# Kernel optimization log

Hardware: AMD Instinct MI355X
Metric: run time of the kernel (lower is better)

## Reference

```python
import jax, jax.numpy as jnp
import numpy as np

N, CAMS = 1, 4
C1, C2, NH = 256, 256, 8
H1, H2, W2 = 128, 64, 400
H, W = 128, 128


def setup_inputs() -> dict:
    key = jax.random.key(0)
    ks = jax.random.split(key, 16)
    sc = 0.02
    th = jax.random.uniform(ks[3], (N, CAMS)) * 2.0 * np.pi
    c, s = jnp.cos(th), jnp.sin(th)
    z, o = jnp.zeros_like(c), jnp.ones_like(c)
    rots = jnp.stack([jnp.stack([c, -s, z], -1), jnp.stack([s, c, z], -1), jnp.stack([z, z, o], -1)], -2)
    return {
        "list_a": jax.random.normal(ks[0], (N, C1, H, W), jnp.float32),
        "list_b": jax.random.normal(ks[1], (N * CAMS, C2, H2, W2), jnp.float32),
        "fov_list": jax.random.uniform(ks[2], (N, CAMS)) * 0.5 + 1.0,
        "rots_list": rots.astype(jnp.float32),
        "trans_list": jax.random.normal(ks[4], (N, CAMS, 3), jnp.float32),
        "fxs": jax.random.uniform(ks[5], (N, CAMS)) * 100.0 + 500.0,
        "cxs": jax.random.uniform(ks[6], (N, CAMS)) * 20.0 + 390.0,
        "pos_a": jax.random.normal(ks[7], (1, H1, C1), jnp.float32),
        "pos_b": jax.random.normal(ks[8], (1, H2, C2), jnp.float32),
        "Wq": jax.random.normal(ks[9], (C1, C1), jnp.float32) * sc,
        "bq": jnp.zeros((C1,), jnp.float32),
        "Wk": jax.random.normal(ks[10], (C1, C2), jnp.float32) * sc,
        "bk": jnp.zeros((C1,), jnp.float32),
        "Wv": jax.random.normal(ks[11], (C1, C2), jnp.float32) * sc,
        "bv": jnp.zeros((C1,), jnp.float32),
        "in_w": jax.random.normal(ks[12], (3 * C1, C1), jnp.float32) * sc,
        "in_b": jnp.zeros((3 * C1,), jnp.float32),
        "out_w": jax.random.normal(ks[13], (C1, C1), jnp.float32) * sc,
        "out_b": jnp.zeros((C1,), jnp.float32),
    }


def _polar_coords(w1, h1, Hh, Ww, rots, fx, cx):
    # per-pixel viewing angles from intrinsics (original image width hard-coded 800)
    pi = jnp.arange(w1, dtype=jnp.float32)
    pw = 800.0 / w1
    ang = jnp.arctan((pi * pw + pw / 2.0 - cx) / fx)
    R90 = jnp.array([[0.0, 1.0], [-1.0, 0.0]], jnp.float32)
    rot = R90 @ rots[:2, :2].astype(jnp.float32)
    cr, sr = rot[0, 0], rot[1, 0]
    ca = cr * jnp.cos(ang) + sr * jnp.sin(ang)
    sa = -sr * jnp.cos(ang) + cr * jnp.sin(ang)
    cxp = jnp.float32(Ww // 2)
    cyp = jnp.float32(Hh // 2)
    rmax = jnp.sqrt(cxp ** 2 + cyp ** 2)
    radii = jnp.linspace(0.0, 1.0, h1).reshape(h1, 1) * rmax
    x = cxp + radii * ca  # [h1, w1]
    y = cyp - radii * sa
    return x, y


def _bilinear(img, x, y):
    # img [C,H,W]; x,y pixel coords [h1,w1]; grid_sample(align_corners=True) after clamping
    Hh, Ww = img.shape[1], img.shape[2]
    x = jnp.clip(x, 0.0, Ww - 1.0)
    y = jnp.clip(y, 0.0, Hh - 1.0)
    x0 = jnp.floor(x); y0 = jnp.floor(y)
    x1 = jnp.clip(x0 + 1.0, 0.0, Ww - 1.0)
    y1 = jnp.clip(y0 + 1.0, 0.0, Hh - 1.0)
    wx = x - x0; wy = y - y0
    x0i, x1i = x0.astype(jnp.int32), x1.astype(jnp.int32)
    y0i, y1i = y0.astype(jnp.int32), y1.astype(jnp.int32)
    v00 = img[:, y0i, x0i]; v01 = img[:, y0i, x1i]
    v10 = img[:, y1i, x0i]; v11 = img[:, y1i, x1i]
    return v00 * (1 - wx) * (1 - wy) + v01 * wx * (1 - wy) + v10 * (1 - wx) * wy + v11 * wx * wy


def _mha(q, k, v, in_w, in_b, out_w, out_b, nh):
    E = q.shape[-1]
    dh = E // nh
    qq = q @ in_w[:E].T + in_b[:E]
    kk = k @ in_w[E:2 * E].T + in_b[E:2 * E]
    vv = v @ in_w[2 * E:].T + in_b[2 * E:]
    B, Lq, _ = q.shape
    Lk = k.shape[1]
    qq = qq.reshape(B, Lq, nh, dh)
    kk = kk.reshape(B, Lk, nh, dh)
    vv = vv.reshape(B, Lk, nh, dh)
    att = jnp.einsum('bqhd,bkhd->bhqk', qq, kk) / jnp.sqrt(jnp.float32(dh))
    p = jax.nn.softmax(att, axis=-1)
    o = jnp.einsum('bhqk,bkhd->bqhd', p, vv).reshape(B, Lq, E)
    return o @ out_w.T + out_b


def _forward(list_a, list_b, rots_list, fxs, cxs, pos_a, pos_b,
             Wq, bq, Wk, bk, Wv, bv, in_w, in_b, out_w, out_b):
    outs = []
    for i in range(list_a.shape[0]):
        a = list_a[i]
        C1_, h1, Wb = a.shape
        Hb = h1
        enh = None
        for j in (0, 3):  # cameras 1 and 2 are skipped by the original `continue`
            b = list_b[i * CAMS + j]
            C2_, h2, w2 = b.shape
            x, y = _polar_coords(w2, h1, a.shape[1], a.shape[2], rots_list[i, j], fxs[i, j], cxs[i, j])
            a_rect = _bilinear(a, x, y)                     # [C1, h1, w2]
            a_seq = jnp.transpose(a_rect, (2, 1, 0)) + pos_a  # [w2, h1, C1]
            b_seq = jnp.transpose(b, (2, 1, 0)) + pos_b       # [w2, h2, C2]
            q = a_seq @ Wq.T + bq
            k = b_seq @ Wk.T + bk
            v = b_seq @ Wv.T + bv
            o = _mha(q, k, v, in_w, in_b, out_w, out_b, NH)
            a_enh = jnp.transpose(o, (2, 1, 0))              # [C1, h1, w2]
            # scatter-add restore with nearest-pixel indices
            xi = jnp.clip(jnp.round(x), 0, a.shape[2] - 1).astype(jnp.int32)
            yi = jnp.clip(jnp.round(y), 0, a.shape[1] - 1).astype(jnp.int32)
            idx = (yi * a.shape[2] + xi).reshape(-1)
            vals = a_enh.reshape(C1_, -1)
            rest = jnp.zeros((C1_, a.shape[1] * a.shape[2]), a.dtype).at[:, idx].add(vals)
            cnt = jnp.zeros((a.shape[1] * a.shape[2],), a.dtype).at[idx].add(1.0)
            cnt = jnp.where(cnt == 0, 1.0, cnt)
            enh = (rest / cnt).reshape(a.shape)
            a = a + enh
        outs.append(a + enh)  # original double-adds the last camera's enhancement
    return jnp.stack(outs)


def reference(list_a, list_b, fov_list, rots_list, trans_list, fxs, cxs, pos_a, pos_b,
              Wq, bq, Wk, bk, Wv, bv, in_w, in_b, out_w, out_b):
    # fov_list / trans_list are accepted but unused in the original math path
    return _forward(list_a, list_b, rots_list, fxs, cxs, pos_a, pos_b,
                    Wq, bq, Wk, bk, Wv, bv, in_w, in_b, out_w, out_b)
```

## Files before the change

### kernel.cpp

```cpp
#include <hip/hip_runtime.h>

#define PIX 16384
#define MS 51200
#define MB 25600

typedef __attribute__((ext_vector_type(8))) short short8;
typedef __attribute__((ext_vector_type(4))) float floatx4;

__device__ inline ushort f2b(float x) {
  uint u = __float_as_uint(x);
  return (ushort)((u + 0x7fffu + ((u >> 16) & 1u)) >> 16);
}
__device__ inline float b2f(ushort u) {
  return __uint_as_float(((uint)u) << 16);
}

__global__ __launch_bounds__(256) void coords_kernel(
    const float* __restrict__ rots, const float* __restrict__ fxs,
    const float* __restrict__ cxs,
    float* __restrict__ xarr, float* __restrict__ yarr,
    int* __restrict__ idxarr, float* __restrict__ cnt)
{
  int jz = blockIdx.y;
  int j = jz ? 3 : 0;
  int s = blockIdx.x * 256 + threadIdx.x;
  int h = s / 400;
  int w = s - h * 400;
  float fx = fxs[j], cx = cxs[j];
  const float* R = rots + j * 9;
  float cr = R[3];
  float sr = -R[0];
  float t = (2.0f * (float)w + 1.0f - cx) / fx;
  float inv = 1.0f / sqrtf(1.0f + t * t);
  float ca = (cr + sr * t) * inv;
  float sa = (cr * t - sr) * inv;
  float rad = ((float)h * (1.0f / 127.0f)) * 90.50966799187808f;
  float x = 64.0f + rad * ca;
  float y = 64.0f - rad * sa;
  xarr[jz * MS + s] = x;
  yarr[jz * MS + s] = y;
  int xi = (int)fminf(fmaxf(rintf(x), 0.0f), 127.0f);
  int yi = (int)fminf(fmaxf(rintf(y), 0.0f), 127.0f);
  int pix = yi * 128 + xi;
  idxarr[jz * MS + s] = pix;
  atomicAdd(&cnt[jz * PIX + pix], 1.0f);
}

__global__ __launch_bounds__(256) void prefix_kernel(
    const float* __restrict__ cntg, int* __restrict__ offsetsg)
{
  const float* cnt = cntg + blockIdx.x * PIX;
  int* offsets = offsetsg + blockIdx.x * PIX;
  __shared__ int sh[256];
  int t = threadIdx.x;
  int base = t * 64;
  const float4* cp = (const float4*)(cnt + base);
  int sum = 0;
#pragma unroll
  for (int i = 0; i < 16; ++i) {
    float4 v = cp[i];
    sum += (int)v.x + (int)v.y + (int)v.z + (int)v.w;
  }
  sh[t] = sum;
  __syncthreads();
  for (int d = 1; d < 256; d <<= 1) {
    int v = (t >= d) ? sh[t - d] : 0;
    __syncthreads();
    sh[t] += v;
    __syncthreads();
  }
  int run = sh[t] - sum;
  int4* op = (int4*)(offsets + base);
#pragma unroll
  for (int i = 0; i < 16; ++i) {
    float4 v = cp[i];
    int a0 = (int)v.x, a1 = (int)v.y, a2 = (int)v.z, a3 = (int)v.w;
    int4 o;
    o.x = run; o.y = run + a0; o.z = run + a0 + a1; o.w = run + a0 + a1 + a2;
    op[i] = o;
    run += a0 + a1 + a2 + a3;
  }
}

__global__ __launch_bounds__(256) void fill_kernel(
    const int* __restrict__ idxarr, const int* __restrict__ offsets,
    int* __restrict__ cursor, int* __restrict__ order, int* __restrict__ pixs)
{
  int jz = blockIdx.y;
  int s = blockIdx.x * 256 + threadIdx.x;
  int pix = idxarr[jz * MS + s];
  int pos = offsets[jz * PIX + pix] + atomicAdd(&cursor[jz * PIX + pix], 1);
  order[jz * MS + pos] = (s % 400) * 128 + (s / 400);
  pixs[jz * MS + pos] = pix;
}

__global__ __launch_bounds__(256) void transpose_kernel(
    const float* __restrict__ src, ushort* __restrict__ dst)
{
  __shared__ float tile[64][65];
  int p0 = blockIdx.x * 64;
  int c0 = blockIdx.y * 64;
  int t = threadIdx.x;
  int pr = (t & 15) * 4;
  int cr = t >> 4;
#pragma unroll
  for (int q = 0; q < 4; ++q) {
    int c = cr + q * 16;
    float4 v = *(const float4*)(src + (size_t)(c0 + c) * PIX + p0 + pr);
    tile[pr + 0][c] = v.x;
    tile[pr + 1][c] = v.y;
    tile[pr + 2][c] = v.z;
    tile[pr + 3][c] = v.w;
  }
  __syncthreads();
  int p = t >> 2;
  int ch = (t & 3) * 16;
  ushort tmp[16];
#pragma unroll
  for (int i = 0; i < 16; ++i) tmp[i] = f2b(tile[p][ch + i]);
  ushort* d = dst + (size_t)(p0 + p) * 256 + c0 + ch;
  *(uint4*)(d) = *(uint4*)tmp;
  *(uint4*)(d + 8) = *(uint4*)(tmp + 8);
}

__global__ __launch_bounds__(256) void f2b_kernel(
    const float* __restrict__ in, ushort* __restrict__ out)
{
  int t = blockIdx.x * 256 + threadIdx.x;
  float4 v = ((const float4*)in)[t];
  ushort4 o;
  o.x = f2b(v.x); o.y = f2b(v.y); o.z = f2b(v.z); o.w = f2b(v.w);
  ((ushort4*)out)[t] = o;
}

#define LFP 264
__global__ __launch_bounds__(256) void sampleproj_kernel(
    const ushort* __restrict__ aT, const float* __restrict__ xarr,
    const float* __restrict__ yarr, const ushort* __restrict__ Wh,
    const float* __restrict__ bias, ushort* __restrict__ qh)
{
  __shared__ ushort lf[64 * LFP];
  int s0 = blockIdx.x * 64;
  int tid = threadIdx.x;
  int lane = tid & 63;
  int wave = tid >> 6;
  int col = lane & 15, quad = lane >> 4;
  int c0 = lane * 4;

#pragma unroll 4
  for (int i = 0; i < 16; ++i) {
    int sl = wave * 16 + i;
    int s = s0 + sl;
    float x = fminf(fmaxf(xarr[s], 0.0f), 127.0f);
    float y = fminf(fmaxf(yarr[s], 0.0f), 127.0f);
    float x0f = floorf(x), y0f = floorf(y);
    int x0 = (int)x0f, y0 = (int)y0f;
    int x1 = min(x0 + 1, 127), y1 = min(y0 + 1, 127);
    float wx = x - x0f, wy = y - y0f;
    float w00 = (1.0f - wx) * (1.0f - wy);
    float w01 = wx * (1.0f - wy);
    float w10 = (1.0f - wx) * wy;
    float w11 = wx * wy;
    ushort4 v00 = *(const ushort4*)(aT + (size_t)(y0 * 128 + x0) * 256 + c0);
    ushort4 v01 = *(const ushort4*)(aT + (size_t)(y0 * 128 + x1) * 256 + c0);
    ushort4 v10 = *(const ushort4*)(aT + (size_t)(y1 * 128 + x0) * 256 + c0);
    ushort4 v11 = *(const ushort4*)(aT + (size_t)(y1 * 128 + x1) * 256 + c0);
    ushort4 o;
    o.x = f2b(w00 * b2f(v00.x) + w01 * b2f(v01.x) + w10 * b2f(v10.x) + w11 * b2f(v11.x));
    o.y = f2b(w00 * b2f(v00.y) + w01 * b2f(v01.y) + w10 * b2f(v10.y) + w11 * b2f(v11.y));
    o.z = f2b(w00 * b2f(v00.z) + w01 * b2f(v01.z) + w10 * b2f(v10.z) + w11 * b2f(v11.z));
    o.w = f2b(w00 * b2f(v00.w) + w01 * b2f(v01.w) + w10 * b2f(v10.w) + w11 * b2f(v11.w));
    *(ushort4*)&lf[sl * LFP + c0] = o;
  }
  __syncthreads();

  int fw = wave * 64;
  floatx4 acc[4][4];
#pragma unroll
  for (int i = 0; i < 4; ++i)
#pragma unroll
    for (int jx = 0; jx < 4; ++jx) acc[i][jx] = (floatx4){0.f, 0.f, 0.f, 0.f};

  for (int kb = 0; kb < 256; kb += 32) {
    short8 aop[4], bop[4];
#pragma unroll
    for (int tf = 0; tf < 4; ++tf)
      aop[tf] = *(const short8*)(Wh + (size_t)(fw + tf * 16 + col) * 256 + kb + quad * 8);
#pragma unroll
    for (int ts = 0; ts < 4; ++ts)
      bop[ts] = *(const short8*)&lf[(ts * 16 + col) * LFP + kb + quad * 8];
#pragma unroll
    for (int ts = 0; ts < 4; ++ts)
#pragma unroll
      for (int tf = 0; tf < 4; ++tf)
        acc[ts][tf] = __builtin_amdgcn_mfma_f32_16x16x32_bf16(
            aop[tf], bop[ts], acc[ts][tf], 0, 0, 0);
  }
#pragma unroll
  for (int ts = 0; ts < 4; ++ts) {
    int s = s0 + ts * 16 + col;
    int h = s / 400;
    int w = s - h * 400;
    size_t obase = (size_t)(w * 128 + h) * 256;
#pragma unroll
    for (int tf = 0; tf < 4; ++tf) {
      int f = fw + tf * 16 + quad * 4;
      float4 bv = *(const float4*)(bias + h * 256 + f);
      ushort4 ov;
      ov.x = f2b(acc[ts][tf][0] + bv.x);
      ov.y = f2b(acc[ts][tf][1] + bv.y);
      ov.z = f2b(acc[ts][tf][2] + bv.z);
      ov.w = f2b(acc[ts][tf][3] + bv.w);
      *(ushort4*)(qh + obase + f) = ov;
    }
  }
}

#define LBP 264
__global__ __launch_bounds__(256) void projKV_kernel(
    const float* __restrict__ bsrc,
    const ushort* __restrict__ WhK, const ushort* __restrict__ WhV,
    const float* __restrict__ biasK, const float* __restrict__ biasV,
    ushort* __restrict__ kh, ushort* __restrict__ vh)
{
  __shared__ ushort lb[64 * LBP];
  int m0 = blockIdx.x * 64;
  int tid = threadIdx.x;
  int lane = tid & 63;
  int wave = tid >> 6;
  int col = lane & 15, quad = lane >> 4;
  int fw = wave * 64;

  int pr = (tid & 15) * 4;
  int cb = tid >> 4;
#pragma unroll 4
  for (int q = 0; q < 16; ++q) {
    int c = cb + q * 16;
    float4 v = *(const float4*)(bsrc + (size_t)c * MB + m0 + pr);
    lb[(pr + 0) * LBP + c] = f2b(v.x);
    lb[(pr + 1) * LBP + c] = f2b(v.y);
    lb[(pr + 2) * LBP + c] = f2b(v.z);
    lb[(pr + 3) * LBP + c] = f2b(v.w);
  }
  __syncthreads();

  floatx4 accK[4][4], accV[4][4];
#pragma unroll
  for (int i = 0; i < 4; ++i)
#pragma unroll
    for (int jx = 0; jx < 4; ++jx) {
      accK[i][jx] = (floatx4){0.f, 0.f, 0.f, 0.f};
      accV[i][jx] = (floatx4){0.f, 0.f, 0.f, 0.f};
    }

  for (int kb = 0; kb < 256; kb += 32) {
    short8 bop[4];
#pragma unroll
    for (int ts = 0; ts < 4; ++ts)
      bop[ts] = *(const short8*)&lb[(ts * 16 + col) * LBP + kb + quad * 8];
    short8 aK[4];
#pragma unroll
    for (int tf = 0; tf < 4; ++tf)
      aK[tf] = *(const short8*)(WhK + (size_t)(fw + tf * 16 + col) * 256 + kb + quad * 8);
#pragma unroll
    for (int ts = 0; ts < 4; ++ts)
#pragma unroll
      for (int tf = 0; tf < 4; ++tf)
        accK[ts][tf] = __builtin_amdgcn_mfma_f32_16x16x32_bf16(
            aK[tf], bop[ts], accK[ts][tf], 0, 0, 0);
    short8 aV[4];
#pragma unroll
    for (int tf = 0; tf < 4; ++tf)
      aV[tf] = *(const short8*)(WhV + (size_t)(fw + tf * 16 + col) * 256 + kb + quad * 8);
#pragma unroll
    for (int ts = 0; ts < 4; ++ts)
#pragma unroll
      for (int tf = 0; tf < 4; ++tf)
        accV[ts][tf] = __builtin_amdgcn_mfma_f32_16x16x32_bf16(
            aV[tf], bop[ts], accV[ts][tf], 0, 0, 0);
  }
#pragma unroll
  for (int ts = 0; ts < 4; ++ts) {
    int m = m0 + ts * 16 + col;
    int h = m / 400;
    int w = m - h * 400;
    size_t obase = (size_t)(w * 64 + h) * 256;
#pragma unroll
    for (int tf = 0; tf < 4; ++tf) {
      int f = fw + tf * 16 + quad * 4;
      float4 bvK = *(const float4*)(biasK + h * 256 + f);
      ushort4 ovK;
      ovK.x = f2b(accK[ts][tf][0] + bvK.x);
      ovK.y = f2b(accK[ts][tf][1] + bvK.y);
      ovK.z = f2b(accK[ts][tf][2] + bvK.z);
      ovK.w = f2b(accK[ts][tf][3] + bvK.w);
      *(ushort4*)(kh + obase + f) = ovK;
      float4 bvV = *(const float4*)(biasV + h * 256 + f);
      ushort4 ovV;
      ovV.x = f2b(accV[ts][tf][0] + bvV.x);
      ovV.y = f2b(accV[ts][tf][1] + bvV.y);
      ovV.z = f2b(accV[ts][tf][2] + bvV.z);
      ovV.w = f2b(accV[ts][tf][3] + bvV.w);
      *(ushort4*)(vh + obase + f) = ovV;
    }
  }
}

#define VP 72
#define PP 72
__global__ __launch_bounds__(256) void attn_mfma_kernel(
    const ushort* __restrict__ qh, const ushort* __restrict__ kh,
    const ushort* __restrict__ vh, ushort* __restrict__ obuf)
{
  __shared__ ushort lV[4][32 * VP];
  __shared__ ushort lP[4][16 * PP];
  int b = blockIdx.x;
  int wave = threadIdx.x >> 6;
  int lane = threadIdx.x & 63;
  int head = blockIdx.y * 4 + wave;
  int col = lane & 15, quad = lane >> 4;
  ushort* Vw = lV[wave];
  ushort* Pw = lP[wave];

  short8 bk0 = *(const short8*)(kh + ((size_t)(b * 64 +  0 + col)) * 256 + head * 32 + quad * 8);
  short8 bk1 = *(const short8*)(kh + ((size_t)(b * 64 + 16 + col)) * 256 + head * 32 + quad * 8);
  short8 bk2 = *(const short8*)(kh + ((size_t)(b * 64 + 32 + col)) * 256 + head * 32 + quad * 8);
  short8 bk3 = *(const short8*)(kh + ((size_t)(b * 64 + 48 + col)) * 256 + head * 32 + quad * 8);

  {
    const ushort* vsrc = vh + ((size_t)(b * 64 + lane)) * 256 + head * 32;
    ushort vr[32];
    *(uint4*)(vr) = *(const uint4*)(vsrc);
    *(uint4*)(vr + 8) = *(const uint4*)(vsrc + 8);
    *(uint4*)(vr + 16) = *(const uint4*)(vsrc + 16);
    *(uint4*)(vr + 24) = *(const uint4*)(vsrc + 24);
#pragma unroll
    for (int d = 0; d < 32; ++d) Vw[d * VP + lane] = vr[d];
  }
  short8 vA0 = *(const short8*)(Vw + (col) * VP + 0 * 32 + quad * 8);
  short8 vB0 = *(const short8*)(Vw + (16 + col) * VP + 0 * 32 + quad * 8);
  short8 vA1 = *(const short8*)(Vw + (col) * VP + 1 * 32 + quad * 8);
  short8 vB1 = *(const short8*)(Vw + (16 + col) * VP + 1 * 32 + quad * 8);

  const float scl = 0.17677669529663687f;
  for (int qt = 0; qt < 8; ++qt) {
    short8 aq = *(const short8*)(qh +
        ((size_t)(b * 128 + qt * 16 + col)) * 256 + head * 32 + quad * 8);
    floatx4 s0 = {0.f,0.f,0.f,0.f}, s1 = s0, s2 = s0, s3 = s0;
    s0 = __builtin_amdgcn_mfma_f32_16x16x32_bf16(aq, bk0, s0, 0, 0, 0);
    s1 = __builtin_amdgcn_mfma_f32_16x16x32_bf16(aq, bk1, s1, 0, 0, 0);
    s2 = __builtin_amdgcn_mfma_f32_16x16x32_bf16(aq, bk2, s2, 0, 0, 0);
    s3 = __builtin_amdgcn_mfma_f32_16x16x32_bf16(aq, bk3, s3, 0, 0, 0);
    float e[4][4], mr[4], sm[4];
#pragma unroll
    for (int r = 0; r < 4; ++r) {
      float v0 = s0[r] * scl, v1 = s1[r] * scl;
      float v2 = s2[r] * scl, v3 = s3[r] * scl;
      e[0][r] = v0; e[1][r] = v1; e[2][r] = v2; e[3][r] = v3;
      mr[r] = fmaxf(fmaxf(v0, v1), fmaxf(v2, v3));
    }
#pragma unroll
    for (int mask = 1; mask <= 8; mask <<= 1)
#pragma unroll
      for (int r = 0; r < 4; ++r)
        mr[r] = fmaxf(mr[r], __shfl_xor(mr[r], mask, 64));
#pragma unroll
    for (int r = 0; r < 4; ++r) {
      float acc = 0.f;
#pragma unroll
      for (int t = 0; t < 4; ++t) {
        float ev = __expf(e[t][r] - mr[r]);
        e[t][r] = ev;
        acc += ev;
      }
      sm[r] = acc;
    }
#pragma unroll
    for (int mask = 1; mask <= 8; mask <<= 1)
#pragma unroll
      for (int r = 0; r < 4; ++r)
        sm[r] += __shfl_xor(sm[r], mask, 64);
#pragma unroll
    for (int t = 0; t < 4; ++t)
#pragma unroll
      for (int r = 0; r < 4; ++r)
        Pw[(quad * 4 + r) * PP + t * 16 + col] = f2b(e[t][r]);
    floatx4 o0 = {0.f,0.f,0.f,0.f}, o1 = o0;
    {
      short8 ap0 = *(const short8*)(Pw + col * PP + 0 * 32 + quad * 8);
      o0 = __builtin_amdgcn_mfma_f32_16x16x32_bf16(ap0, vA0, o0, 0, 0, 0);
      o1 = __builtin_amdgcn_mfma_f32_16x16x32_bf16(ap0, vB0, o1, 0, 0, 0);
      short8 ap1 = *(const short8*)(Pw + col * PP + 1 * 32 + quad * 8);
      o0 = __builtin_amdgcn_mfma_f32_16x16x32_bf16(ap1, vA1, o0, 0, 0, 0);
      o1 = __builtin_amdgcn_mfma_f32_16x16x32_bf16(ap1, vB1, o1, 0, 0, 0);
    }
#pragma unroll
    for (int r = 0; r < 4; ++r) {
      float iv = 1.0f / sm[r];
      size_t row = (size_t)(b * 128 + qt * 16 + quad * 4 + r) * 256 + head * 32;
      obuf[row + col] = f2b(o0[r] * iv);
      obuf[row + 16 + col] = f2b(o1[r] * iv);
    }
  }
}

__global__ __launch_bounds__(256) void gemmN3_kernel(
    const float* __restrict__ pos_a, const float* __restrict__ pos_b,
    const float* __restrict__ weff, const float* __restrict__ beff,
    float* __restrict__ qpos, float* __restrict__ kpos, float* __restrict__ vpos)
{
  int z = blockIdx.z;
  if (z > 0 && blockIdx.x > 0) return;
  const float* A = (z == 0) ? pos_a : pos_b;
  const float* Wt = weff + (size_t)z * 65536;
  const float* biasf = beff + z * 256;
  float* Cout = (z == 0) ? qpos : ((z == 1) ? kpos : vpos);
  __shared__ float As[64][17];
  __shared__ float Ws[16][65];
  int m0 = blockIdx.x * 64;
  int n0 = blockIdx.y * 64;
  int tid = threadIdx.x;
  int tx = tid & 15, ty = tid >> 4;
  float acc[4][4] = {};
  for (int k0 = 0; k0 < 256; k0 += 16) {
    {
      int m = tid >> 2;
      int kq = (tid & 3) << 2;
      float4 v = *(const float4*)(A + (size_t)(m0 + m) * 256 + k0 + kq);
      As[m][kq + 0] = v.x; As[m][kq + 1] = v.y;
      As[m][kq + 2] = v.z; As[m][kq + 3] = v.w;
    }
    {
      int f = tid >> 2;
      int kq = (tid & 3) << 2;
      float4 v = *(const float4*)(Wt + (size_t)(n0 + f) * 256 + k0 + kq);
      Ws[kq + 0][f] = v.x; Ws[kq + 1][f] = v.y;
      Ws[kq + 2][f] = v.z; Ws[kq + 3][f] = v.w;
    }
    __syncthreads();
#pragma unroll
    for (int kk = 0; kk < 16; ++kk) {
      float a[4], b[4];
#pragma unroll
      for (int i = 0; i < 4; ++i) a[i] = As[ty * 4 + i][kk];
#pragma unroll
      for (int jj = 0; jj < 4; ++jj) b[jj] = Ws[kk][tx * 4 + jj];
#pragma unroll
      for (int i = 0; i < 4; ++i)
#pragma unroll
        for (int jj = 0; jj < 4; ++jj) acc[i][jj] += a[i] * b[jj];
    }
    __syncthreads();
  }
#pragma unroll
  for (int i = 0; i < 4; ++i) {
    int m = m0 + ty * 4 + i;
    int f = n0 + tx * 4;
    float4 bv = *(const float4*)(biasf + f);
    float4 ov;
    ov.x = acc[i][0] + bv.x; ov.y = acc[i][1] + bv.y;
    ov.z = acc[i][2] + bv.z; ov.w = acc[i][3] + bv.w;
    *(float4*)(Cout + (size_t)m * 256 + f) = ov;
  }
}

__global__ __launch_bounds__(256) void gemm_ab_kernel(
    const float* __restrict__ in_w, const float* __restrict__ Wq,
    const float* __restrict__ Wk, const float* __restrict__ Wv,
    float* __restrict__ weff, ushort* __restrict__ weffh)
{
  int z = blockIdx.z;
  const float* A = in_w + (size_t)z * 65536;
  const float* B = (z == 0) ? Wq : ((z == 1) ? Wk : Wv);
  float* C = weff + (size_t)z * 65536;
  ushort* Ch = weffh + (size_t)z * 65536;
  __shared__ float As[64][17];
  __shared__ float Bs[16][64];
  int m0 = blockIdx.x * 64;
  int n0 = blockIdx.y * 64;
  int tid = threadIdx.x;
  int tx = tid & 15, ty = tid >> 4;
  float acc[4][4] = {};
  for (int k0 = 0; k0 < 256; k0 += 16) {
    {
      int m = tid >> 2;
      int kq = (tid & 3) << 2;
      float4 v = *(const float4*)(A + (size_t)(m0 + m) * 256 + k0 + kq);
      As[m][kq + 0] = v.x; As[m][kq + 1] = v.y;
      As[m][kq + 2] = v.z; As[m][kq + 3] = v.w;
    }
    {
      int k = tid >> 4;
      int nq = (tid & 15) << 2;
      float4 v = *(const float4*)(B + (size_t)(k0 + k) * 256 + n0 + nq);
      *(float4*)(&Bs[k][nq]) = v;
    }
    __syncthreads();
#pragma unroll
    for (int kk = 0; kk < 16; ++kk) {
      float a[4], b[4];
#pragma unroll
      for (int i = 0; i < 4; ++i) a[i] = As[ty * 4 + i][kk];
#pragma unroll
      for (int jj = 0; jj < 4; ++jj) b[jj] = Bs[kk][tx * 4 + jj];
#pragma unroll
      for (int i = 0; i < 4; ++i)
#pragma unroll
        for (int jj = 0; jj < 4; ++jj) acc[i][jj] += a[i] * b[jj];
    }
    __syncthreads();
  }
#pragma unroll
  for (int i = 0; i < 4; ++i) {
    int m = m0 + ty * 4 + i;
    *(float4*)(C + (size_t)m * 256 + n0 + tx * 4) = *(float4*)&acc[i][0];
    ushort4 hv;
    hv.x = f2b(acc[i][0]); hv.y = f2b(acc[i][1]);
    hv.z = f2b(acc[i][2]); hv.w = f2b(acc[i][3]);
    *(ushort4*)(Ch + (size_t)m * 256 + n0 + tx * 4) = hv;
  }
}

__global__ void beff_kernel(const float* __restrict__ in_w, const float* __restrict__ in_b,
                            const float* __restrict__ bq, const float* __restrict__ bk,
                            const float* __restrict__ bv, float* __restrict__ beff)
{
  int z = blockIdx.x;
  int f = threadIdx.x;
  const float* bsrc = (z == 0) ? bq : ((z == 1) ? bk : bv);
  const float* row = in_w + (size_t)(z * 256 + f) * 256;
  float acc = in_b[z * 256 + f];
  for (int e = 0; e < 256; ++e) acc += row[e] * bsrc[e];
  beff[z * 256 + f] = acc;
}

#define CH 64
__global__ __launch_bounds__(256) void segred_kernel(
    const ushort* __restrict__ obuf, const int* __restrict__ order,
    const int* __restrict__ pixs, float* __restrict__ osum)
{
  __shared__ int lm[CH];
  __shared__ int lp[CH + 2];
  int s0 = blockIdx.x * CH;
  int t = threadIdx.x;
  if (t < CH) {
    lm[t] = order[s0 + t];
    lp[t + 1] = pixs[s0 + t];
  } else if (t == CH) {
    lp[0] = (s0 > 0) ? pixs[s0 - 1] : -1;
  } else if (t == CH + 1) {
    lp[CH + 1] = (s0 + CH < MS) ? pixs[s0 + CH] : -2;
  }
  __syncthreads();
  int c = t;
  float va[8];
#pragma unroll
  for (int k = 0; k < 8; ++k)
    va[k] = b2f(obuf[(size_t)lm[k] * 256 + c]);
  float acc = 0.0f;
  int runBegin = 0;
#pragma unroll
  for (int i = 0; i < CH; ++i) {
    float v = va[i & 7];
    if (i + 8 < CH) va[i & 7] = b2f(obuf[(size_t)lm[i + 8] * 256 + c]);
    acc += v;
    int p = lp[i + 1];
    bool last = (i == CH - 1);
    if (last || p != lp[i + 2]) {
      bool pBeg = (runBegin == 0) && (p == lp[0]);
      bool pEnd = last && (p == lp[CH + 1]);
      float* dst = osum + (size_t)p * 256 + c;
      if (pBeg || pEnd) atomicAdd(dst, acc);
      else *dst = acc;
      acc = 0.0f;
      runBegin = i + 1;
    }
  }
}

__global__ __launch_bounds__(256) void outproj_update_kernel(
    const float* __restrict__ osum, const ushort* __restrict__ out_wh,
    const float* __restrict__ asrc, float* __restrict__ adst,
    const float* __restrict__ cnt, const float* __restrict__ out_b,
    float scale, ushort* __restrict__ aTout, int writeAT)
{
  int p0 = blockIdx.x * 64;
  int lane = threadIdx.x & 63;
  int wave = threadIdx.x >> 6;
  int col = lane & 15, quad = lane >> 4;
  int fw = wave * 64;
  floatx4 acc[4][4];
#pragma unroll
  for (int i = 0; i < 4; ++i)
#pragma unroll
    for (int jx = 0; jx < 4; ++jx) acc[i][jx] = (floatx4){0.f, 0.f, 0.f, 0.f};

  for (int kb = 0; kb < 256; kb += 32) {
    short8 aop[4], bop[4];
#pragma unroll
    for (int tf = 0; tf < 4; ++tf)
      aop[tf] = *(const short8*)(out_wh +
          (size_t)(fw + tf * 16 + col) * 256 + kb + quad * 8);
#pragma unroll
    for (int ts = 0; ts < 4; ++ts) {
      const float* brow = osum + (size_t)(p0 + ts * 16 + col) * 256 + kb + quad * 8;
      float4 f0 = *(const float4*)brow;
      float4 f1 = *(const float4*)(brow + 4);
      short8 bv;
      bv[0] = (short)f2b(f0.x); bv[1] = (short)f2b(f0.y);
      bv[2] = (short)f2b(f0.z); bv[3] = (short)f2b(f0.w);
      bv[4] = (short)f2b(f1.x); bv[5] = (short)f2b(f1.y);
      bv[6] = (short)f2b(f1.z); bv[7] = (short)f2b(f1.w);
      bop[ts] = bv;
    }
#pragma unroll
    for (int ts = 0; ts < 4; ++ts)
#pragma unroll
      for (int tf = 0; tf < 4; ++tf)
        acc[ts][tf] = __builtin_amdgcn_mfma_f32_16x16x32_bf16(
            aop[tf], bop[ts], acc[ts][tf], 0, 0, 0);
  }
#pragma unroll
  for (int ts = 0; ts < 4; ++ts) {
    int p = p0 + ts * 16 + col;
    float cn = cnt[p];
    float rs = scale / fmaxf(cn, 1.0f);
#pragma unroll
    for (int tf = 0; tf < 4; ++tf) {
      int f = fw + tf * 16 + quad * 4;
      float4 ob = *(const float4*)(out_b + f);
      float r0 = asrc[(size_t)(f + 0) * PIX + p] + (acc[ts][tf][0] + cn * ob.x) * rs;
      float r1 = asrc[(size_t)(f + 1) * PIX + p] + (acc[ts][tf][1] + cn * ob.y) * rs;
      float r2 = asrc[(size_t)(f + 2) * PIX + p] + (acc[ts][tf][2] + cn * ob.z) * rs;
      float r3 = asrc[(size_t)(f + 3) * PIX + p] + (acc[ts][tf][3] + cn * ob.w) * rs;
      adst[(size_t)(f + 0) * PIX + p] = r0;
      adst[(size_t)(f + 1) * PIX + p] = r1;
      adst[(size_t)(f + 2) * PIX + p] = r2;
      adst[(size_t)(f + 3) * PIX + p] = r3;
      if (writeAT) {
        ushort4 hv;
        hv.x = f2b(r0); hv.y = f2b(r1); hv.z = f2b(r2); hv.w = f2b(r3);
        *(ushort4*)(aTout + (size_t)p * 256 + f) = hv;
      }
    }
  }
}

extern "C" void kernel_launch(void* const* d_in, const int* in_sizes, int n_in,
                              void* d_out, int out_size, void* d_ws, size_t ws_size,
                              hipStream_t stream) {
  const float* list_a = (const float*)d_in[0];
  const float* list_b = (const float*)d_in[1];
  const float* rots   = (const float*)d_in[3];
  const float* fxs    = (const float*)d_in[5];
  const float* cxs    = (const float*)d_in[6];
  const float* pos_a  = (const float*)d_in[7];
  const float* pos_b  = (const float*)d_in[8];
  const float* Wq     = (const float*)d_in[9];
  const float* bq     = (const float*)d_in[10];
  const float* Wk     = (const float*)d_in[11];
  const float* bk     = (const float*)d_in[12];
  const float* Wv     = (const float*)d_in[13];
  const float* bv     = (const float*)d_in[14];
  const float* in_w   = (const float*)d_in[15];
  const float* in_b   = (const float*)d_in[16];
  const float* out_w  = (const float*)d_in[17];
  const float* out_b  = (const float*)d_in[18];

  float* ws      = (float*)d_ws;
  float* weff    = ws;
  float* beff    = weff + 196608;
  float* qpos    = beff + 768;
  float* kpos    = qpos + 32768;
  float* vpos    = kpos + 16384;
  float* a_cur   = vpos + 16384;
  float* xarr    = a_cur + 4194304;
  float* yarr    = xarr + 102400;
  int*   idxarr  = (int*)(yarr + 102400);
  int*   offs    = idxarr + 102400;
  int*   order   = offs + 32768;
  int*   pixs    = order + 102400;
  float* cnt     = (float*)(pixs + 102400);
  int*   cursor  = (int*)(cnt + 32768);
  float* osum    = (float*)(cursor + 32768);
  ushort* weffh  = (ushort*)(osum + 4194304);
  ushort* out_wh = weffh + 196608;
  ushort* obufh  = out_wh + 65536;
  ushort* qh     = obufh + 13107200;
  ushort* kh     = qh + 13107200;
  ushort* vh     = kh + 6553600;
  ushort* aT     = vh + 6553600;

  gemm_ab_kernel<<<dim3(4, 4, 3), 256, 0, stream>>>(in_w, Wq, Wk, Wv, weff, weffh);
  beff_kernel<<<3, 256, 0, stream>>>(in_w, in_b, bq, bk, bv, beff);
  f2b_kernel<<<64, 256, 0, stream>>>(out_w, out_wh);
  gemmN3_kernel<<<dim3(2, 4, 3), 256, 0, stream>>>(pos_a, pos_b, weff, beff,
                                                   qpos, kpos, vpos);
  hipMemsetAsync(cnt, 0, (size_t)(32768 + 32768) * sizeof(float), stream);
  coords_kernel<<<dim3(200, 2), 256, 0, stream>>>(rots, fxs, cxs, xarr, yarr, idxarr, cnt);
  prefix_kernel<<<2, 256, 0, stream>>>(cnt, offs);
  fill_kernel<<<dim3(200, 2), 256, 0, stream>>>(idxarr, offs, cursor, order, pixs);

  for (int jj = 0; jj < 2; ++jj) {
    int j = jj ? 3 : 0;
    const float* asrc = jj ? a_cur : list_a;
    hipMemsetAsync(osum, 0, (size_t)4194304 * sizeof(float), stream);
    if (jj == 0)
      transpose_kernel<<<dim3(256, 4), 256, 0, stream>>>(list_a, aT);
    sampleproj_kernel<<<800, 256, 0, stream>>>(aT, xarr + jj * MS, yarr + jj * MS,
                                               weffh, qpos, qh);
    projKV_kernel<<<400, 256, 0, stream>>>(list_b + (size_t)j * 6553600,
                                           weffh + 65536, weffh + 131072,
                                           kpos, vpos, kh, vh);
    attn_mfma_kernel<<<dim3(400, 2), 256, 0, stream>>>(qh, kh, vh, obufh);
    segred_kernel<<<800, 256, 0, stream>>>(obufh, order + jj * MS, pixs + jj * MS, osum);
    outproj_update_kernel<<<256, 256, 0, stream>>>(osum, out_wh, asrc,
                                                   jj ? (float*)d_out : a_cur,
                                                   cnt + jj * PIX, out_b,
                                                   jj ? 2.0f : 1.0f,
                                                   aT, jj == 0 ? 1 : 0);
  }
}
```

Baseline: 560.7 us.

## Merge projection kernels, split attention query tiles, halve outproj tile, coalesce attn stores

Fuses the Q sample-projection and K/V projection kernels into one launch with a block-index branch, and merges the bias and weight-conversion setup kernels into one. Attention blocks now handle half the query tiles each, doubling the grid. Outputs are staged through LDS so each row goes out as one 16-byte store instead of scattered 2-byte stores. The out-projection tile shrinks from 64 to 32 pixels, doubling its block count. The aim is fewer launches and more parallel work to fill the GPU, at the cost of reloading K/V per attention block and reloading weights per out-projection block.

```diff
diff --git a/kernel.cpp b/kernel.cpp
--- a/kernel.cpp
+++ b/kernel.cpp
@@ -123,24 +123,37 @@
   *(uint4*)(d + 8) = *(uint4*)(tmp + 8);
 }
 
-__global__ __launch_bounds__(256) void f2b_kernel(
-    const float* __restrict__ in, ushort* __restrict__ out)
-{
-  int t = blockIdx.x * 256 + threadIdx.x;
-  float4 v = ((const float4*)in)[t];
-  ushort4 o;
-  o.x = f2b(v.x); o.y = f2b(v.y); o.z = f2b(v.z); o.w = f2b(v.w);
-  ((ushort4*)out)[t] = o;
+__global__ __launch_bounds__(256) void misc_kernel(
+    const float* __restrict__ out_w, ushort* __restrict__ out_wh,
+    const float* __restrict__ in_w, const float* __restrict__ in_b,
+    const float* __restrict__ bq, const float* __restrict__ bk,
+    const float* __restrict__ bv, float* __restrict__ beff)
+{
+  if (blockIdx.x < 64) {
+    int t = blockIdx.x * 256 + threadIdx.x;
+    float4 v = ((const float4*)out_w)[t];
+    ushort4 o;
+    o.x = f2b(v.x); o.y = f2b(v.y); o.z = f2b(v.z); o.w = f2b(v.w);
+    ((ushort4*)out_wh)[t] = o;
+  } else {
+    int z = blockIdx.x - 64;
+    int f = threadIdx.x;
+    const float* bsrc = (z == 0) ? bq : ((z == 1) ? bk : bv);
+    const float* row = in_w + (size_t)(z * 256 + f) * 256;
+    float acc = in_b[z * 256 + f];
+    for (int e = 0; e < 256; ++e) acc += row[e] * bsrc[e];
+    beff[z * 256 + f] = acc;
+  }
 }
 
 #define LFP 264
-__global__ __launch_bounds__(256) void sampleproj_kernel(
+__device__ __forceinline__ void sampleproj_body(
+    ushort* lf, int bx,
     const ushort* __restrict__ aT, const float* __restrict__ xarr,
     const float* __restrict__ yarr, const ushort* __restrict__ Wh,
     const float* __restrict__ bias, ushort* __restrict__ qh)
 {
-  __shared__ ushort lf[64 * LFP];
-  int s0 = blockIdx.x * 64;
+  int s0 = bx * 64;
   int tid = threadIdx.x;
   int lane = tid & 63;
   int wave = tid >> 6;
@@ -216,15 +229,14 @@
   }
 }
 
-#define LBP 264
-__global__ __launch_bounds__(256) void projKV_kernel(
+__device__ __forceinline__ void projKV_body(
+    ushort* lb, int bx,
     const float* __restrict__ bsrc,
     const ushort* __restrict__ WhK, const ushort* __restrict__ WhV,
     const float* __restrict__ biasK, const float* __restrict__ biasV,
     ushort* __restrict__ kh, ushort* __restrict__ vh)
 {
-  __shared__ ushort lb[64 * LBP];
-  int m0 = blockIdx.x * 64;
+  int m0 = bx * 64;
   int tid = threadIdx.x;
   int lane = tid & 63;
   int wave = tid >> 6;
@@ -237,10 +249,10 @@
   for (int q = 0; q < 16; ++q) {
     int c = cb + q * 16;
     float4 v = *(const float4*)(bsrc + (size_t)c * MB + m0 + pr);
-    lb[(pr + 0) * LBP + c] = f2b(v.x);
-    lb[(pr + 1) * LBP + c] = f2b(v.y);
-    lb[(pr + 2) * LBP + c] = f2b(v.z);
-    lb[(pr + 3) * LBP + c] = f2b(v.w);
+    lb[(pr + 0) * LFP + c] = f2b(v.x);
+    lb[(pr + 1) * LFP + c] = f2b(v.y);
+    lb[(pr + 2) * LFP + c] = f2b(v.z);
+    lb[(pr + 3) * LFP + c] = f2b(v.w);
   }
   __syncthreads();
 
@@ -257,7 +269,7 @@
     short8 bop[4];
 #pragma unroll
     for (int ts = 0; ts < 4; ++ts)
-      bop[ts] = *(const short8*)&lb[(ts * 16 + col) * LBP + kb + quad * 8];
+      bop[ts] = *(const short8*)&lb[(ts * 16 + col) * LFP + kb + quad * 8];
     short8 aK[4];
 #pragma unroll
     for (int tf = 0; tf < 4; ++tf)
@@ -306,6 +318,22 @@
   }
 }
 
+__global__ __launch_bounds__(256) void proj_kernel(
+    const ushort* __restrict__ aT, const float* __restrict__ xarr,
+    const float* __restrict__ yarr, const ushort* __restrict__ weffh,
+    const float* __restrict__ qpos, ushort* __restrict__ qh,
+    const float* __restrict__ bsrc,
+    const float* __restrict__ kpos, const float* __restrict__ vpos,
+    ushort* __restrict__ kh, ushort* __restrict__ vh)
+{
+  __shared__ ushort lf[64 * LFP];
+  if (blockIdx.x < 800)
+    sampleproj_body(lf, blockIdx.x, aT, xarr, yarr, weffh, qpos, qh);
+  else
+    projKV_body(lf, blockIdx.x - 800, bsrc, weffh + 65536, weffh + 131072,
+                kpos, vpos, kh, vh);
+}
+
 #define VP 72
 #define PP 72
 __global__ __launch_bounds__(256) void attn_mfma_kernel(
@@ -315,9 +343,11 @@
   __shared__ ushort lV[4][32 * VP];
   __shared__ ushort lP[4][16 * PP];
   int b = blockIdx.x;
+  int hg = blockIdx.y & 1;
+  int qb = blockIdx.y >> 1;
   int wave = threadIdx.x >> 6;
   int lane = threadIdx.x & 63;
-  int head = blockIdx.y * 4 + wave;
+  int head = hg * 4 + wave;
   int col = lane & 15, quad = lane >> 4;
   ushort* Vw = lV[wave];
   ushort* Pw = lP[wave];
@@ -343,7 +373,7 @@
   short8 vB1 = *(const short8*)(Vw + (16 + col) * VP + 1 * 32 + quad * 8);
 
   const float scl = 0.17677669529663687f;
-  for (int qt = 0; qt < 8; ++qt) {
+  for (int qt = qb * 4; qt < qb * 4 + 4; ++qt) {
     short8 aq = *(const short8*)(qh +
         ((size_t)(b * 128 + qt * 16 + col)) * 256 + head * 32 + quad * 8);
     floatx4 s0 = {0.f,0.f,0.f,0.f}, s1 = s0, s2 = s0, s3 = s0;
@@ -397,10 +427,12 @@
 #pragma unroll
     for (int r = 0; r < 4; ++r) {
       float iv = 1.0f / sm[r];
-      size_t row = (size_t)(b * 128 + qt * 16 + quad * 4 + r) * 256 + head * 32;
-      obuf[row + col] = f2b(o0[r] * iv);
-      obuf[row + 16 + col] = f2b(o1[r] * iv);
-    }
+      Pw[(quad * 4 + r) * PP + col] = f2b(o0[r] * iv);
+      Pw[(quad * 4 + r) * PP + 16 + col] = f2b(o1[r] * iv);
+    }
+    int orow = lane >> 2, ochunk = lane & 3;
+    uint4 ov = *(const uint4*)(Pw + orow * PP + ochunk * 8);
+    *(uint4*)(obuf + (size_t)(b * 128 + qt * 16 + orow) * 256 + head * 32 + ochunk * 8) = ov;
   }
 }
 
@@ -521,19 +553,6 @@
   }
 }
 
-__global__ void beff_kernel(const float* __restrict__ in_w, const float* __restrict__ in_b,
-                            const float* __restrict__ bq, const float* __restrict__ bk,
-                            const float* __restrict__ bv, float* __restrict__ beff)
-{
-  int z = blockIdx.x;
-  int f = threadIdx.x;
-  const float* bsrc = (z == 0) ? bq : ((z == 1) ? bk : bv);
-  const float* row = in_w + (size_t)(z * 256 + f) * 256;
-  float acc = in_b[z * 256 + f];
-  for (int e = 0; e < 256; ++e) acc += row[e] * bsrc[e];
-  beff[z * 256 + f] = acc;
-}
-
 #define CH 64
 __global__ __launch_bounds__(256) void segred_kernel(
     const ushort* __restrict__ obuf, const int* __restrict__ order,
@@ -584,25 +603,25 @@
     const float* __restrict__ cnt, const float* __restrict__ out_b,
     float scale, ushort* __restrict__ aTout, int writeAT)
 {
-  int p0 = blockIdx.x * 64;
+  int p0 = blockIdx.x * 32;
   int lane = threadIdx.x & 63;
   int wave = threadIdx.x >> 6;
   int col = lane & 15, quad = lane >> 4;
   int fw = wave * 64;
-  floatx4 acc[4][4];
-#pragma unroll
-  for (int i = 0; i < 4; ++i)
+  floatx4 acc[2][4];
+#pragma unroll
+  for (int i = 0; i < 2; ++i)
 #pragma unroll
     for (int jx = 0; jx < 4; ++jx) acc[i][jx] = (floatx4){0.f, 0.f, 0.f, 0.f};
 
   for (int kb = 0; kb < 256; kb += 32) {
-    short8 aop[4], bop[4];
+    short8 aop[4], bop[2];
 #pragma unroll
     for (int tf = 0; tf < 4; ++tf)
       aop[tf] = *(const short8*)(out_wh +
           (size_t)(fw + tf * 16 + col) * 256 + kb + quad * 8);
 #pragma unroll
-    for (int ts = 0; ts < 4; ++ts) {
+    for (int ts = 0; ts < 2; ++ts) {
       const float* brow = osum + (size_t)(p0 + ts * 16 + col) * 256 + kb + quad * 8;
       float4 f0 = *(const float4*)brow;
       float4 f1 = *(const float4*)(brow + 4);
@@ -614,14 +633,14 @@
       bop[ts] = bv;
     }
 #pragma unroll
-    for (int ts = 0; ts < 4; ++ts)
+    for (int ts = 0; ts < 2; ++ts)
 #pragma unroll
       for (int tf = 0; tf < 4; ++tf)
         acc[ts][tf] = __builtin_amdgcn_mfma_f32_16x16x32_bf16(
             aop[tf], bop[ts], acc[ts][tf], 0, 0, 0);
   }
 #pragma unroll
-  for (int ts = 0; ts < 4; ++ts) {
+  for (int ts = 0; ts < 2; ++ts) {
     int p = p0 + ts * 16 + col;
     float cn = cnt[p];
     float rs = scale / fmaxf(cn, 1.0f);
@@ -692,8 +711,7 @@
   ushort* aT     = vh + 6553600;
 
   gemm_ab_kernel<<<dim3(4, 4, 3), 256, 0, stream>>>(in_w, Wq, Wk, Wv, weff, weffh);
-  beff_kernel<<<3, 256, 0, stream>>>(in_w, in_b, bq, bk, bv, beff);
-  f2b_kernel<<<64, 256, 0, stream>>>(out_w, out_wh);
+  misc_kernel<<<67, 256, 0, stream>>>(out_w, out_wh, in_w, in_b, bq, bk, bv, beff);
   gemmN3_kernel<<<dim3(2, 4, 3), 256, 0, stream>>>(pos_a, pos_b, weff, beff,
                                                    qpos, kpos, vpos);
   hipMemsetAsync(cnt, 0, (size_t)(32768 + 32768) * sizeof(float), stream);
@@ -707,14 +725,13 @@
     hipMemsetAsync(osum, 0, (size_t)4194304 * sizeof(float), stream);
     if (jj == 0)
       transpose_kernel<<<dim3(256, 4), 256, 0, stream>>>(list_a, aT);
-    sampleproj_kernel<<<800, 256, 0, stream>>>(aT, xarr + jj * MS, yarr + jj * MS,
-                                               weffh, qpos, qh);
-    projKV_kernel<<<400, 256, 0, stream>>>(list_b + (size_t)j * 6553600,
-                                           weffh + 65536, weffh + 131072,
-                                           kpos, vpos, kh, vh);
-    attn_mfma_kernel<<<dim3(400, 2), 256, 0, stream>>>(qh, kh, vh, obufh);
+    proj_kernel<<<1200, 256, 0, stream>>>(aT, xarr + jj * MS, yarr + jj * MS,
+                                          weffh, qpos, qh,
+                                          list_b + (size_t)j * 6553600,
+                                          kpos, vpos, kh, vh);
+    attn_mfma_kernel<<<dim3(400, 4), 256, 0, stream>>>(qh, kh, vh, obufh);
     segred_kernel<<<800, 256, 0, stream>>>(obufh, order + jj * MS, pixs + jj * MS, osum);
-    outproj_update_kernel<<<256, 256, 0, stream>>>(osum, out_wh, asrc,
+    outproj_update_kernel<<<512, 256, 0, stream>>>(osum, out_wh, asrc,
                                                    jj ? (float*)d_out : a_cur,
                                                    cnt + jj * PIX, out_b,
                                                    jj ? 2.0f : 1.0f,
```

Measured after the change: 557.9 us. Within noise of the previous version (-0.5%).
